# Optimization experiments

Hardware: AMD Instinct MI355X
Metric: run time of the kernel (lower is better)

## Reference

```python
import jax, jax.numpy as jnp
import numpy as np

N, DIM, K = 131072, 64, 1024


def setup_inputs() -> dict:
    key = jax.random.key(0)
    kx, ke = jax.random.split(key)
    x = jax.random.normal(kx, (N, DIM), dtype=jnp.float32)
    # codebook buffer, initialized like uniform(-1/K, 1/K) in the original
    scale = 1.0 / K
    embedding = jax.random.uniform(ke, (K, DIM), dtype=jnp.float32, minval=-scale, maxval=scale)
    return {"x": x, "embedding": embedding}


def reference(x, embedding):
    # squared euclidean distances in fp32 (matches compute_distances)
    x32 = x.astype(jnp.float32)
    e32 = embedding.astype(jnp.float32)
    distances = (
        jnp.sum(x32 * x32, axis=1, keepdims=True)
        + jnp.sum(e32 * e32, axis=1)
        - 2.0 * jnp.einsum("nd,kd->nk", x32, e32)
    )
    indices = jnp.argmin(distances, axis=1)          # (N,)
    quantized = embedding[indices]                    # (N, DIM) codebook gather
    # commitment loss: mse(stop_grad(quantized), x)
    commitment_loss = jnp.mean((jax.lax.stop_gradient(quantized) - x) ** 2)
    # straight-through estimator
    quantized_st = x + jax.lax.stop_gradient(quantized - x)
    return quantized_st, indices, commitment_loss
```

## Files before the change

kernel.cpp:

```cpp
#include <hip/hip_runtime.h>
#include <hip/hip_bf16.h>

#define N_ROWS 131072
#define DIM 64
#define K_CODES 1024
#define NTILES 64
#define MARGIN 4e-5f
#define LIST_CAP 65536

typedef short short8 __attribute__((ext_vector_type(8)));
typedef float f32x4 __attribute__((ext_vector_type(4)));

__device__ __forceinline__ unsigned short f2bf(float f) {
    unsigned u = __float_as_uint(f);
    return (unsigned short)((u + 0x7fffu + ((u >> 16) & 1u)) >> 16);
}
__device__ __forceinline__ float bf2f(unsigned short h) {
    return __uint_as_float(((unsigned)h) << 16);
}

__device__ __forceinline__ float np_sq64(const float* __restrict__ v) {
    float xx[DIM];
    #pragma unroll
    for (int d = 0; d < DIM; ++d) xx[d] = v[d] * v[d];
    float r[8];
    #pragma unroll
    for (int j = 0; j < 8; ++j) r[j] = xx[j];
    #pragma unroll
    for (int i = 8; i < DIM; i += 8)
        #pragma unroll
        for (int j = 0; j < 8; ++j) r[j] = r[j] + xx[i + j];
    return ((r[0]+r[1]) + (r[2]+r[3])) + ((r[4]+r[5]) + (r[6]+r[7]));
}

__device__ __forceinline__ float np_dot64(const float* __restrict__ xv,
                                          const float* __restrict__ ek) {
    float a0 = 0.f, a1 = 0.f, a2 = 0.f, a3 = 0.f;
    #pragma unroll
    for (int c = 0; c < DIM; c += 16)
        #pragma unroll
        for (int b = 12; b >= 0; b -= 4) {
            const int d = c + b;
            a0 = a0 + xv[d+0] * ek[d+0];
            a1 = a1 + xv[d+1] * ek[d+1];
            a2 = a2 + xv[d+2] * ek[d+2];
            a3 = a3 + xv[d+3] * ek[d+3];
        }
    return (a0 + a1) + (a2 + a3);
}


__global__ void vq_prep(const float* __restrict__ emb, float* __restrict__ esq,
                        unsigned short* __restrict__ wsB,
                        unsigned int* __restrict__ cnt, float* __restrict__ loss) {
#pragma clang fp contract(off)
    const int t = blockIdx.x * blockDim.x + threadIdx.x;
    if (t == 0) { *cnt = 0u; *loss = 0.f; }
    const int k = t >> 2, c = t & 3;
    if (k >= K_CODES) return;
    const float* e = emb + (size_t)k * DIM;

    if (c == 0) esq[k] = np_sq64(e);

    const int off = (c & 1) * 32, sel = c >> 1;
    unsigned short val[32];
    #pragma unroll
    for (int j = 0; j < 32; ++j) {
        float v = e[off + j];
        unsigned short h = f2bf(v);
        val[j] = sel ? f2bf(v - bf2f(h)) : h;
    }
    const int tile = k >> 4, n = k & 15;
    #pragma unroll
    for (int g = 0; g < 4; ++g) {
        short8 s;
        #pragma unroll
        for (int j = 0; j < 8; ++j) s[j] = (short)val[g*8 + j];
        *reinterpret_cast<short8*>(wsB + ((size_t)((tile*4 + c)*64 + g*16 + n)) * 8) = s;
    }
}

__global__ __launch_bounds__(256, 2) void vq_mfma(const float* __restrict__ x,
        const float* __restrict__ emb, const float* __restrict__ esq,
        const unsigned short* __restrict__ wsB, float* __restrict__ out,
        unsigned int* __restrict__ cnt, unsigned int* __restrict__ list,
        float* __restrict__ loss) {
#pragma clang fp contract(off)
    const int tid = threadIdx.x;
    const int lane = tid & 63;
    const int w = tid >> 6;
    const int g = lane >> 4, res = lane & 15;
    const int rowbase = blockIdx.x * 256 + w * 64;

    auto loadB = [&](short8* Bd, int ct) {
        const unsigned short* bp = wsB + ((size_t)(ct*4)*64 + lane) * 8;
        #pragma unroll
        for (int c = 0; c < 4; ++c)
            Bd[c] = *reinterpret_cast<const short8*>(bp + (size_t)c * 64 * 8);
    };

    short8 B0[4], B1[4], B2[4], B3[4];
    loadB(B0, 0); loadB(B1, 1); loadB(B2, 2); loadB(B3, 3);
    float e0 = esq[res], e1 = esq[16 + res];

    short8 Ah[4][2], Al[4][2];
    #pragma unroll
    for (int rg = 0; rg < 4; ++rg) {
        const float* xr = x + (size_t)(rowbase + rg*16 + res) * DIM;
        #pragma unroll
        for (int h = 0; h < 2; ++h) {
            float4 v0 = *reinterpret_cast<const float4*>(xr + h*32 + g*8);
            float4 v1 = *reinterpret_cast<const float4*>(xr + h*32 + g*8 + 4);
            float xv[8] = {v0.x, v0.y, v0.z, v0.w, v1.x, v1.y, v1.z, v1.w};
            short8 sh, sl;
            #pragma unroll
            for (int j = 0; j < 8; ++j) {
                unsigned short hb = f2bf(xv[j]);
                sh[j] = (short)hb;
                sl[j] = (short)f2bf(xv[j] - bf2f(hb));
            }
            Ah[rg][h] = sh; Al[rg][h] = sl;
        }
    }

    float b1[16], b2[16], b3[16], b4[16];
    const float FINF = __uint_as_float(0x7F800000u);
    #pragma unroll
    for (int s = 0; s < 16; ++s) { b1[s]=FINF; b2[s]=FINF; b3[s]=FINF; b4[s]=FINF; }

    auto MF = [&](f32x4* acc, const short8* B) {
        __builtin_amdgcn_s_setprio(1);
        #pragma unroll
        for (int rg = 0; rg < 4; ++rg) acc[rg] = f32x4{0.f, 0.f, 0.f, 0.f};
        #pragma unroll
        for (int rg = 0; rg < 4; ++rg)
            acc[rg] = __builtin_amdgcn_mfma_f32_16x16x32_bf16(Ah[rg][0], B[0], acc[rg], 0,0,0);
        #pragma unroll
        for (int rg = 0; rg < 4; ++rg)
            acc[rg] = __builtin_amdgcn_mfma_f32_16x16x32_bf16(Ah[rg][1], B[1], acc[rg], 0,0,0);
        #pragma unroll
        for (int rg = 0; rg < 4; ++rg)
            acc[rg] = __builtin_amdgcn_mfma_f32_16x16x32_bf16(Ah[rg][0], B[2], acc[rg], 0,0,0);
        #pragma unroll
        for (int rg = 0; rg < 4; ++rg)
            acc[rg] = __builtin_amdgcn_mfma_f32_16x16x32_bf16(Ah[rg][1], B[3], acc[rg], 0,0,0);
        #pragma unroll
        for (int rg = 0; rg < 4; ++rg)
            acc[rg] = __builtin_amdgcn_mfma_f32_16x16x32_bf16(Al[rg][0], B[0], acc[rg], 0,0,0);
        #pragma unroll
        for (int rg = 0; rg < 4; ++rg)
            acc[rg] = __builtin_amdgcn_mfma_f32_16x16x32_bf16(Al[rg][1], B[1], acc[rg], 0,0,0);
        __builtin_amdgcn_s_setprio(0);
    };

    auto KY = [&](const f32x4* acc, float esqv, int ct) {
        const unsigned kcur = (unsigned)(ct*16 + res);
        #pragma unroll
        for (int rg = 0; rg < 4; ++rg) {
            #pragma unroll
            for (int r = 0; r < 4; ++r) {
                float v = fmaf(-2.0f, acc[rg][r], esqv);
                float key = __uint_as_float((__float_as_uint(v) & 0xFFFFFC00u) | kcur);
                const int s = rg*4 + r;
                float o1 = b1[s], o2 = b2[s], o3 = b3[s];
                b4[s] = __builtin_amdgcn_fmed3f(key, o3, b4[s]);
                b3[s] = __builtin_amdgcn_fmed3f(key, o2, o3);
                b2[s] = __builtin_amdgcn_fmed3f(key, o1, o2);
                b1[s] = fminf(o1, key);
            }
        }
    };

    f32x4 accA[4], accB[4];
    MF(accA, B0);
    for (int p = 0; p < 15; ++p) {
        const int t = 4 * p;
        loadB(B0, t + 4);
        MF(accB, B1);
        KY(accA, e0, t);      e0 = esq[(t + 2) * 16 + res];
        loadB(B1, t + 5);
        MF(accA, B2);
        KY(accB, e1, t + 1);  e1 = esq[(t + 3) * 16 + res];
        loadB(B2, t + 6);
        MF(accB, B3);
        KY(accA, e0, t + 2);  e0 = esq[(t + 4) * 16 + res];
        loadB(B3, t + 7);
        MF(accA, B0);
        KY(accB, e1, t + 3);  e1 = esq[(t + 5) * 16 + res];
    }
    MF(accB, B1);
    KY(accA, e0, 60);  e0 = esq[62 * 16 + res];
    MF(accA, B2);
    KY(accB, e1, 61);  e1 = esq[63 * 16 + res];
    MF(accB, B3);
    KY(accA, e0, 62);
    KY(accB, e1, 63);

    #pragma unroll
    for (int m = 1; m < 16; m <<= 1) {
        #pragma unroll
        for (int s = 0; s < 16; ++s) {
            float oa1 = __shfl_xor(b1[s], m, 64);
            float oa2 = __shfl_xor(b2[s], m, 64);
            float oa3 = __shfl_xor(b3[s], m, 64);
            float oa4 = __shfl_xor(b4[s], m, 64);
            float m1 = fminf(b1[s], oa1);
            float m2 = fminf(fmaxf(b1[s], oa1), fminf(b2[s], oa2));
            float m3 = fminf(fminf(fmaxf(b1[s], oa2), fmaxf(b2[s], oa1)),
                             fminf(b3[s], oa3));
            float m4 = fminf(fminf(fmaxf(b1[s], oa3), fmaxf(b3[s], oa1)),
                             fminf(fmaxf(b2[s], oa2), fminf(b4[s], oa4)));
            b1[s] = m1; b2[s] = m2; b3[s] = m3; b4[s] = m4;
        }
    }

    __shared__ float s_k1[256], s_k2[256], s_k3[256], s_k4[256];
    __shared__ int s_idx[256];
    if (res == 0) {
        #pragma unroll
        for (int s = 0; s < 16; ++s) {
            const int rl = w*64 + (s >> 2)*16 + g*4 + (s & 3);
            s_k1[rl] = b1[s]; s_k2[rl] = b2[s]; s_k3[rl] = b3[s]; s_k4[rl] = b4[s];
        }
    }
    __syncthreads();

    {
        const int row = blockIdx.x * 256 + tid;
        unsigned u1 = __float_as_uint(s_k1[tid]);
        unsigned u2 = __float_as_uint(s_k2[tid]);
        unsigned u3 = __float_as_uint(s_k3[tid]);
        unsigned u4 = __float_as_uint(s_k4[tid]);
        float f1 = __uint_as_float(u1 & 0xFFFFFC00u);
        float f2 = __uint_as_float(u2 & 0xFFFFFC00u);
        float f3 = __uint_as_float(u3 & 0xFFFFFC00u);
        float f4 = __uint_as_float(u4 & 0xFFFFFC00u);
        int idx;
        if (f4 - f1 < MARGIN) {
            unsigned slot = atomicAdd(cnt, 1u);
            if (slot < LIST_CAP) list[slot] = (unsigned)row;
            idx = -1;
        } else if (f2 - f1 < MARGIN) {
            const int nc = (f3 - f1 < MARGIN) ? 3 : 2;
            int cand[3] = {(int)(u1 & 0x3FFu), (int)(u2 & 0x3FFu), (int)(u3 & 0x3FFu)};
            float xv[DIM];
            const float4* xp = reinterpret_cast<const float4*>(x + (size_t)row * DIM);
            #pragma unroll
            for (int q = 0; q < 16; ++q) {
                float4 v = xp[q];
                xv[4*q+0] = v.x; xv[4*q+1] = v.y; xv[4*q+2] = v.z; xv[4*q+3] = v.w;
            }
            float xsq = np_sq64(xv);
            float bd = INFINITY; int bi = 0x7fffffff;
            for (int c = 0; c < nc; ++c) {
                const int k = cand[c];
                float tt = xsq + esq[k];
                float dd = tt - 2.0f * np_dot64(xv, emb + (size_t)k * DIM);
                if (dd < bd || (dd == bd && k < bi)) { bd = dd; bi = k; }
            }
            idx = bi;
        } else {
            idx = (int)(u1 & 0x3FFu);
        }
        s_idx[tid] = idx;
    }
    __syncthreads();

    float lsum = 0.f;
    #pragma unroll
    for (int pass = 0; pass < 2; ++pass) {
        const int rl = (tid >> 1) + pass * 128, half = tid & 1;
        const int row = blockIdx.x * 256 + rl;
        const int idx = s_idx[rl];
        if (idx >= 0) {
            const float* xr = x + (size_t)row * DIM + half*32;
            const float* qr = emb + (size_t)idx * DIM + half*32;
            float* orow = out + (size_t)row * DIM + half*32;
            #pragma unroll
            for (int i = 0; i < 8; ++i) {
                float4 xv = reinterpret_cast<const float4*>(xr)[i];
                float4 qv = reinterpret_cast<const float4*>(qr)[i];
                float df0 = qv.x - xv.x, df1 = qv.y - xv.y;
                float df2 = qv.z - xv.z, df3 = qv.w - xv.w;
                lsum = fmaf(df0, df0, lsum); lsum = fmaf(df1, df1, lsum);
                lsum = fmaf(df2, df2, lsum); lsum = fmaf(df3, df3, lsum);
                float4 o = {xv.x + df0, xv.y + df1, xv.z + df2, xv.w + df3};
                reinterpret_cast<float4*>(orow)[i] = o;
            }
            if (half == 0) out[(size_t)N_ROWS * DIM + row] = (float)idx;
        }
    }
    #pragma unroll
    for (int off = 32; off > 0; off >>= 1) lsum += __shfl_down(lsum, off, 64);
    if (lane == 0) atomicAdd(loss, lsum);
}

__global__ void vq_fixup(const float* __restrict__ x, const float* __restrict__ emb,
                         const float* __restrict__ esq,
                         const unsigned int* __restrict__ cnt,
                         const unsigned int* __restrict__ list,
                         float* __restrict__ out, float* __restrict__ loss) {
#pragma clang fp contract(off)
    const int lane = threadIdx.x & 63;
    const int wid = (blockIdx.x * blockDim.x + threadIdx.x) >> 6;
    const int nw = (256 * 256) >> 6;
    unsigned count = *cnt;
    if (count > LIST_CAP) count = LIST_CAP;
    for (unsigned i = wid; i < count; i += nw) {
        const int row = (int)list[i];
        float xv[DIM];
        const float4* xp = reinterpret_cast<const float4*>(x + (size_t)row * DIM);
        #pragma unroll
        for (int q = 0; q < 16; ++q) {
            float4 v = xp[q];
            xv[4*q+0] = v.x; xv[4*q+1] = v.y; xv[4*q+2] = v.z; xv[4*q+3] = v.w;
        }
        float xsq = np_sq64(xv);
        float best = INFINITY; int bidx = 0x7fffffff;
        for (int t = 0; t < K_CODES / 64; ++t) {
            const int k = lane + t * 64;
            float dot = np_dot64(xv, emb + (size_t)k * DIM);
            float tt = xsq + esq[k];
            float dist = tt - 2.0f * dot;
            if (dist < best) { best = dist; bidx = k; }
        }
        #pragma unroll
        for (int m = 1; m < 64; m <<= 1) {
            float ob = __shfl_xor(best, m, 64);
            int   oi = __shfl_xor(bidx, m, 64);
            if (ob < best || (ob == best && oi < bidx)) { best = ob; bidx = oi; }
        }
        const float xd = x[(size_t)row * DIM + lane];
        const float qd = emb[(size_t)bidx * DIM + lane];
        const float df = qd - xd;
        out[(size_t)row * DIM + lane] = xd + df;
        if (lane == 0) out[(size_t)N_ROWS * DIM + row] = (float)bidx;
        float l2 = df * df;
        #pragma unroll
        for (int off = 32; off > 0; off >>= 1) l2 += __shfl_down(l2, off, 64);
        if (lane == 0) atomicAdd(loss, l2);
    }
}

__global__ void vq_final(const float* __restrict__ loss_acc, float* __restrict__ out_loss) {
    if (threadIdx.x == 0 && blockIdx.x == 0)
        out_loss[0] = loss_acc[0] / (float)((size_t)N_ROWS * DIM);
}

extern "C" void kernel_launch(void* const* d_in, const int* in_sizes, int n_in,
                              void* d_out, int out_size, void* d_ws, size_t ws_size,
                              hipStream_t stream) {
    const float* x   = (const float*)d_in[0];
    const float* emb = (const float*)d_in[1];
    float* out = (float*)d_out;

    unsigned int* cnt  = (unsigned int*)d_ws;
    float* loss        = (float*)d_ws + 1;
    float* esq         = (float*)d_ws + 4;
    unsigned short* wsB = (unsigned short*)((char*)d_ws + 8192);
    unsigned int* list = (unsigned int*)((char*)d_ws + 270336);

    vq_prep<<<dim3(64), dim3(64), 0, stream>>>(emb, esq, wsB, cnt, loss);
    vq_mfma<<<dim3(N_ROWS / 256), dim3(256), 0, stream>>>(x, emb, esq, wsB, out,
                                                          cnt, list, loss);
    vq_fixup<<<dim3(256), dim3(256), 0, stream>>>(x, emb, esq, cnt, list, out, loss);
    vq_final<<<dim3(1), dim3(1), 0, stream>>>(loss, out + (size_t)N_ROWS * DIM + N_ROWS);
}
```

Measured before the change: 130.9 us.

## Split MFMA accumulators into two chains, widen fixup grid, fold final kernel

Each distance tile's MFMA sequence now alternates between two independent accumulator sets, which are summed before key formation. This halves the dependent MFMA chain length and allows more back-to-back issue, at the cost of extra accumulator registers and one add per element. The fixup kernel launches twice as many blocks, and the separate loss-finalisation kernel is removed. In its place, the last fixup block to finish (tracked by an atomic counter) writes the mean loss, saving one kernel launch.

```diff
diff --git a/kernel.cpp b/kernel.cpp
--- a/kernel.cpp
+++ b/kernel.cpp
@@ -7,6 +7,7 @@
 #define NTILES 64
 #define MARGIN 4e-5f
 #define LIST_CAP 65536
+#define FIX_BLOCKS 512
 
 typedef short short8 __attribute__((ext_vector_type(8)));
 typedef float f32x4 __attribute__((ext_vector_type(4)));
@@ -52,10 +53,11 @@
 
 __global__ void vq_prep(const float* __restrict__ emb, float* __restrict__ esq,
                         unsigned short* __restrict__ wsB,
-                        unsigned int* __restrict__ cnt, float* __restrict__ loss) {
+                        unsigned int* __restrict__ cnt, float* __restrict__ loss,
+                        unsigned int* __restrict__ done) {
 #pragma clang fp contract(off)
     const int t = blockIdx.x * blockDim.x + threadIdx.x;
-    if (t == 0) { *cnt = 0u; *loss = 0.f; }
+    if (t == 0) { *cnt = 0u; *loss = 0.f; *done = 0u; }
     const int k = t >> 2, c = t & 3;
     if (k >= K_CODES) return;
     const float* e = emb + (size_t)k * DIM;
@@ -128,38 +130,38 @@
     #pragma unroll
     for (int s = 0; s < 16; ++s) { b1[s]=FINF; b2[s]=FINF; b3[s]=FINF; b4[s]=FINF; }
 
-    auto MF = [&](f32x4* acc, const short8* B) {
+    auto MF = [&](f32x4* aX, f32x4* aY, const short8* B) {
         __builtin_amdgcn_s_setprio(1);
         #pragma unroll
-        for (int rg = 0; rg < 4; ++rg) acc[rg] = f32x4{0.f, 0.f, 0.f, 0.f};
-        #pragma unroll
-        for (int rg = 0; rg < 4; ++rg)
-            acc[rg] = __builtin_amdgcn_mfma_f32_16x16x32_bf16(Ah[rg][0], B[0], acc[rg], 0,0,0);
-        #pragma unroll
-        for (int rg = 0; rg < 4; ++rg)
-            acc[rg] = __builtin_amdgcn_mfma_f32_16x16x32_bf16(Ah[rg][1], B[1], acc[rg], 0,0,0);
-        #pragma unroll
-        for (int rg = 0; rg < 4; ++rg)
-            acc[rg] = __builtin_amdgcn_mfma_f32_16x16x32_bf16(Ah[rg][0], B[2], acc[rg], 0,0,0);
-        #pragma unroll
-        for (int rg = 0; rg < 4; ++rg)
-            acc[rg] = __builtin_amdgcn_mfma_f32_16x16x32_bf16(Ah[rg][1], B[3], acc[rg], 0,0,0);
-        #pragma unroll
-        for (int rg = 0; rg < 4; ++rg)
-            acc[rg] = __builtin_amdgcn_mfma_f32_16x16x32_bf16(Al[rg][0], B[0], acc[rg], 0,0,0);
-        #pragma unroll
-        for (int rg = 0; rg < 4; ++rg)
-            acc[rg] = __builtin_amdgcn_mfma_f32_16x16x32_bf16(Al[rg][1], B[1], acc[rg], 0,0,0);
+        for (int rg = 0; rg < 4; ++rg) { aX[rg] = f32x4{0.f,0.f,0.f,0.f}; aY[rg] = f32x4{0.f,0.f,0.f,0.f}; }
+        #pragma unroll
+        for (int rg = 0; rg < 4; ++rg)
+            aX[rg] = __builtin_amdgcn_mfma_f32_16x16x32_bf16(Ah[rg][0], B[0], aX[rg], 0,0,0);
+        #pragma unroll
+        for (int rg = 0; rg < 4; ++rg)
+            aY[rg] = __builtin_amdgcn_mfma_f32_16x16x32_bf16(Ah[rg][1], B[1], aY[rg], 0,0,0);
+        #pragma unroll
+        for (int rg = 0; rg < 4; ++rg)
+            aX[rg] = __builtin_amdgcn_mfma_f32_16x16x32_bf16(Ah[rg][0], B[2], aX[rg], 0,0,0);
+        #pragma unroll
+        for (int rg = 0; rg < 4; ++rg)
+            aY[rg] = __builtin_amdgcn_mfma_f32_16x16x32_bf16(Ah[rg][1], B[3], aY[rg], 0,0,0);
+        #pragma unroll
+        for (int rg = 0; rg < 4; ++rg)
+            aX[rg] = __builtin_amdgcn_mfma_f32_16x16x32_bf16(Al[rg][0], B[0], aX[rg], 0,0,0);
+        #pragma unroll
+        for (int rg = 0; rg < 4; ++rg)
+            aY[rg] = __builtin_amdgcn_mfma_f32_16x16x32_bf16(Al[rg][1], B[1], aY[rg], 0,0,0);
         __builtin_amdgcn_s_setprio(0);
     };
 
-    auto KY = [&](const f32x4* acc, float esqv, int ct) {
+    auto KY = [&](const f32x4* aX, const f32x4* aY, float esqv, int ct) {
         const unsigned kcur = (unsigned)(ct*16 + res);
         #pragma unroll
         for (int rg = 0; rg < 4; ++rg) {
             #pragma unroll
             for (int r = 0; r < 4; ++r) {
-                float v = fmaf(-2.0f, acc[rg][r], esqv);
+                float v = fmaf(-2.0f, aX[rg][r] + aY[rg][r], esqv);
                 float key = __uint_as_float((__float_as_uint(v) & 0xFFFFFC00u) | kcur);
                 const int s = rg*4 + r;
                 float o1 = b1[s], o2 = b2[s], o3 = b3[s];
@@ -171,30 +173,30 @@
         }
     };
 
-    f32x4 accA[4], accB[4];
-    MF(accA, B0);
+    f32x4 aX[4], aY[4], bX[4], bY[4];
+    MF(aX, aY, B0);
     for (int p = 0; p < 15; ++p) {
         const int t = 4 * p;
         loadB(B0, t + 4);
-        MF(accB, B1);
-        KY(accA, e0, t);      e0 = esq[(t + 2) * 16 + res];
+        MF(bX, bY, B1);
+        KY(aX, aY, e0, t);      e0 = esq[(t + 2) * 16 + res];
         loadB(B1, t + 5);
-        MF(accA, B2);
-        KY(accB, e1, t + 1);  e1 = esq[(t + 3) * 16 + res];
+        MF(aX, aY, B2);
+        KY(bX, bY, e1, t + 1);  e1 = esq[(t + 3) * 16 + res];
         loadB(B2, t + 6);
-        MF(accB, B3);
-        KY(accA, e0, t + 2);  e0 = esq[(t + 4) * 16 + res];
+        MF(bX, bY, B3);
+        KY(aX, aY, e0, t + 2);  e0 = esq[(t + 4) * 16 + res];
         loadB(B3, t + 7);
-        MF(accA, B0);
-        KY(accB, e1, t + 3);  e1 = esq[(t + 5) * 16 + res];
-    }
-    MF(accB, B1);
-    KY(accA, e0, 60);  e0 = esq[62 * 16 + res];
-    MF(accA, B2);
-    KY(accB, e1, 61);  e1 = esq[63 * 16 + res];
-    MF(accB, B3);
-    KY(accA, e0, 62);
-    KY(accB, e1, 63);
+        MF(aX, aY, B0);
+        KY(bX, bY, e1, t + 3);  e1 = esq[(t + 5) * 16 + res];
+    }
+    MF(bX, bY, B1);
+    KY(aX, aY, e0, 60);  e0 = esq[62 * 16 + res];
+    MF(aX, aY, B2);
+    KY(bX, bY, e1, 61);  e1 = esq[63 * 16 + res];
+    MF(bX, bY, B3);
+    KY(aX, aY, e0, 62);
+    KY(bX, bY, e1, 63);
 
     #pragma unroll
     for (int m = 1; m < 16; m <<= 1) {
@@ -299,11 +301,12 @@
                          const float* __restrict__ esq,
                          const unsigned int* __restrict__ cnt,
                          const unsigned int* __restrict__ list,
-                         float* __restrict__ out, float* __restrict__ loss) {
+                         float* __restrict__ out, float* __restrict__ loss,
+                         unsigned int* __restrict__ done) {
 #pragma clang fp contract(off)
     const int lane = threadIdx.x & 63;
     const int wid = (blockIdx.x * blockDim.x + threadIdx.x) >> 6;
-    const int nw = (256 * 256) >> 6;
+    const int nw = (FIX_BLOCKS * 256) >> 6;
     unsigned count = *cnt;
     if (count > LIST_CAP) count = LIST_CAP;
     for (unsigned i = wid; i < count; i += nw) {
@@ -340,11 +343,16 @@
         for (int off = 32; off > 0; off >>= 1) l2 += __shfl_down(l2, off, 64);
         if (lane == 0) atomicAdd(loss, l2);
     }
-}
-
-__global__ void vq_final(const float* __restrict__ loss_acc, float* __restrict__ out_loss) {
-    if (threadIdx.x == 0 && blockIdx.x == 0)
-        out_loss[0] = loss_acc[0] / (float)((size_t)N_ROWS * DIM);
+
+    __syncthreads();
+    __threadfence();
+    if (threadIdx.x == 0) {
+        unsigned d = atomicAdd(done, 1u);
+        if (d == (unsigned)(FIX_BLOCKS - 1)) {
+            float total = atomicAdd(loss, 0.0f);
+            out[(size_t)N_ROWS * DIM + N_ROWS] = total / (float)((size_t)N_ROWS * DIM);
+        }
+    }
 }
 
 extern "C" void kernel_launch(void* const* d_in, const int* in_sizes, int n_in,
@@ -356,13 +364,14 @@
 
     unsigned int* cnt  = (unsigned int*)d_ws;
     float* loss        = (float*)d_ws + 1;
+    unsigned int* done = (unsigned int*)d_ws + 2;
     float* esq         = (float*)d_ws + 4;
     unsigned short* wsB = (unsigned short*)((char*)d_ws + 8192);
     unsigned int* list = (unsigned int*)((char*)d_ws + 270336);
 
-    vq_prep<<<dim3(64), dim3(64), 0, stream>>>(emb, esq, wsB, cnt, loss);
+    vq_prep<<<dim3(64), dim3(64), 0, stream>>>(emb, esq, wsB, cnt, loss, done);
     vq_mfma<<<dim3(N_ROWS / 256), dim3(256), 0, stream>>>(x, emb, esq, wsB, out,
                                                           cnt, list, loss);
-    vq_fixup<<<dim3(256), dim3(256), 0, stream>>>(x, emb, esq, cnt, list, out, loss);
-    vq_final<<<dim3(1), dim3(1), 0, stream>>>(loss, out + (size_t)N_ROWS * DIM + N_ROWS);
-}
+    vq_fixup<<<dim3(FIX_BLOCKS), dim3(256), 0, stream>>>(x, emb, esq, cnt, list,
+                                                         out, loss, done);
+}
```

New measurement: 282.4 us. 2.16x slower.
